# Performance work log

Hardware: AMD Instinct MI355X
Metric: run time of the kernel (lower is better)

## Reference

```python
import jax, jax.numpy as jnp
import numpy as np

B, LQ, LKV = 2, 2048, 1024
DQ = DK = DV_IN = 512
H, DQK, DV = 8, 64, 64
DOUT = 512
SPAN, STRIDE = 128, 2


def setup_inputs() -> dict:
    key = jax.random.key(0)
    ks = jax.random.split(key, 7)
    W_SCALE = 0.05  # keep pre-softmax logits in a sane range
    return {
        "q": jax.random.normal(ks[0], (B, LQ, DQ), jnp.float32),
        "k": jax.random.normal(ks[1], (B, LKV, DK), jnp.float32),
        "v": jax.random.normal(ks[2], (B, LKV, DV_IN), jnp.float32),
        "Wq": jax.random.normal(ks[3], (DQ, H * DQK), jnp.float32) * W_SCALE,
        "Wk": jax.random.normal(ks[4], (DK, H * DQK), jnp.float32) * W_SCALE,
        "Wv": jax.random.normal(ks[5], (DV_IN, H * DV), jnp.float32) * W_SCALE,
        "Wout": jax.random.normal(ks[6], (H * DV, DOUT), jnp.float32) * W_SCALE,
        "head_num": H,
        "span": SPAN,
        "stride": STRIDE,
    }


def reference(q, k, v, Wq, Wk, Wv, Wout, head_num, span, stride):
    batch, length_q, _ = q.shape
    length_kv = k.shape[1]
    width = -(-span // stride)  # ceil(span / stride)
    hd_qk = Wq.shape[1] // head_num
    hd_v = Wv.shape[1] // head_num

    Q = (q @ Wq).reshape(batch, length_q, head_num, hd_qk)
    K = (k @ Wk).reshape(batch, length_kv, head_num, hd_qk)
    V = (v @ Wv).reshape(batch, length_kv, head_num, hd_v)

    # Local-window indices: query j attends kv position j//stride + w - (width-1)
    j = jnp.arange(length_q)[:, None]            # [Lq, 1]
    w = jnp.arange(width)[None, :]               # [1, width]
    orig_col = w - (width - 1) + j // stride     # [Lq, width]
    valid = (orig_col >= 0) & (orig_col < length_kv) & \
            ((j % stride) <= span - 1 - (width - w - 1) * stride)
    mask = jnp.where(valid, 0.0, -jnp.inf).astype(q.dtype)
    idx = jnp.clip(orig_col, 0, length_kv - 1)   # masked entries are dont-care

    Kg = K[:, idx]                               # [B, Lq, width, H, dQK]
    # NOTE: original module applies NO 1/sqrt(d) scaling
    scores = jnp.einsum('bjhd,bjwhd->bhjw', Q, Kg) + mask[None, None]
    p = jax.nn.softmax(scores, axis=-1)          # [B, H, Lq, width]

    Vg = V[:, idx]                               # [B, Lq, width, H, dV]
    out = jnp.einsum('bhjw,bjwhd->bjhd', p, Vg)
    out = out.reshape(batch, length_q, head_num * hd_v)
    return out @ Wout
```

## Files before the change

### kernel.cpp

```cpp
#include <hip/hip_runtime.h>
#include <stdint.h>

typedef _Float16 f16;
typedef _Float16 f16x8 __attribute__((ext_vector_type(8)));
typedef float f32x4 __attribute__((ext_vector_type(4)));

#define LQn   2048
#define LKVn  1024
#define DM    512
#define NH    8

static __device__ __forceinline__ f32x4 mfma_f16(f16x8 a, f16x8 b, f32x4 c) {
  return __builtin_amdgcn_mfma_f32_16x16x32_f16(a, b, c, 0, 0, 0);
}

__global__ __launch_bounds__(256) void transpose_w_kernel(
    const float* __restrict__ Wq, const float* __restrict__ Wk,
    const float* __restrict__ Wv, const float* __restrict__ Wo,
    f16* __restrict__ WT) {
  __shared__ float tile[64 * 65];
  const int bid = blockIdx.x;
  const int mat = bid >> 6;
  const int tb  = bid & 63;
  const int r0 = (tb >> 3) * 64;
  const int c0 = (tb & 7) * 64;
  const float* W = (mat == 0) ? Wq : (mat == 1) ? Wk : (mat == 2) ? Wv : Wo;
  const int t = threadIdx.x;
#pragma unroll
  for (int i = 0; i < 16; ++i) {
    int idx = i * 256 + t;
    int r = idx >> 6, c = idx & 63;
    tile[r * 65 + c] = W[(size_t)(r0 + r) * DM + c0 + c];
  }
  __syncthreads();
#pragma unroll
  for (int i = 0; i < 16; ++i) {
    int idx = i * 256 + t;
    int r = idx >> 6, c = idx & 63;
    WT[(size_t)mat * DM * DM + (size_t)(c0 + r) * DM + r0 + c] =
        (f16)tile[c * 65 + r];
  }
}

__device__ __forceinline__ void proj_tile(const float* __restrict__ Ap,
                                          const f16* __restrict__ Bp,
                                          f16* __restrict__ C,
                                          int m0, int n0,
                                          f16* smA, f16* smB) {
  const int t = threadIdx.x;
  const int lane = t & 63;
  const int w = t >> 6;
  const int ln = lane & 15, hi4 = lane >> 4;
  const int wr = w >> 2, wc = w & 3;
  const f32x4 zf = {0.f, 0.f, 0.f, 0.f};
  f32x4 acc[4][2];
#pragma unroll
  for (int a = 0; a < 4; ++a)
#pragma unroll
    for (int b = 0; b < 2; ++b) acc[a][b] = zf;

  for (int k0 = 0; k0 < 512; k0 += 64) {
    f16x8 av[2], bv[2];
#pragma unroll
    for (int i = 0; i < 2; ++i) {
      int idx = i * 512 + t;
      int r = idx >> 3, u = idx & 7;
      const float* g = Ap + (size_t)(m0 + r) * 512 + k0 + u * 8;
      f32x4 x0 = *(const f32x4*)g, x1 = *(const f32x4*)(g + 4);
      f16x8 hv;
#pragma unroll
      for (int e = 0; e < 4; ++e) { hv[e] = (f16)x0[e]; hv[4 + e] = (f16)x1[e]; }
      av[i] = hv;
      bv[i] = *(const f16x8*)(Bp + (size_t)(n0 + r) * 512 + k0 + u * 8);
    }
    __syncthreads();
#pragma unroll
    for (int i = 0; i < 2; ++i) {
      int idx = i * 512 + t;
      int r = idx >> 3, u = idx & 7;
      int sw = r * 64 + ((u ^ (r & 7)) * 8);
      *(f16x8*)&smA[sw] = av[i];
      *(f16x8*)&smB[sw] = bv[i];
    }
    __syncthreads();
#pragma unroll
    for (int kk = 0; kk < 64; kk += 32) {
      const int ub = kk >> 3;
      f16x8 ah[4], bh[2];
#pragma unroll
      for (int mf = 0; mf < 4; ++mf) {
        int row = wr * 64 + mf * 16 + ln;
        ah[mf] = *(const f16x8*)&smA[row * 64 + (((ub + hi4) ^ (ln & 7)) * 8)];
      }
#pragma unroll
      for (int nf = 0; nf < 2; ++nf) {
        int row = wc * 32 + nf * 16 + ln;
        bh[nf] = *(const f16x8*)&smB[row * 64 + (((ub + hi4) ^ (ln & 7)) * 8)];
      }
#pragma unroll
      for (int mf = 0; mf < 4; ++mf)
#pragma unroll
        for (int nf = 0; nf < 2; ++nf)
          acc[mf][nf] = mfma_f16(ah[mf], bh[nf], acc[mf][nf]);
    }
  }
#pragma unroll
  for (int mf = 0; mf < 4; ++mf)
#pragma unroll
    for (int nf = 0; nf < 2; ++nf)
#pragma unroll
      for (int e = 0; e < 4; ++e) {
        size_t off = (size_t)(m0 + wr * 64 + mf * 16 + hi4 * 4 + e) * 512 +
                     n0 + wc * 32 + nf * 16 + ln;
        C[off] = (f16)acc[mf][nf][e];
      }
}

__global__ __launch_bounds__(512, 2) void proj_kernel(
    const float* __restrict__ q, const float* __restrict__ k,
    const float* __restrict__ v, const f16* __restrict__ WT,
    f16* __restrict__ Qf, f16* __restrict__ Kf, f16* __restrict__ Vf) {
  __shared__ f16 smA[128 * 64];
  __shared__ f16 smB[128 * 64];
  const int bid = blockIdx.x;
  if (bid < 128) {
    int m0 = (bid >> 2) * 128, n0 = (bid & 3) * 128;
    proj_tile(q, WT, Qf, m0, n0, smA, smB);
  } else if (bid < 192) {
    int b2 = bid - 128;
    int m0 = (b2 >> 2) * 128, n0 = (b2 & 3) * 128;
    proj_tile(k, WT + (size_t)DM * DM, Kf, m0, n0, smA, smB);
  } else {
    int b2 = bid - 192;
    int m0 = (b2 >> 2) * 128, n0 = (b2 & 3) * 128;
    proj_tile(v, WT + (size_t)2 * DM * DM, Vf, m0, n0, smA, smB);
  }
}

__global__ __launch_bounds__(256) void outproj_kernel(
    const f16* __restrict__ AO, const f16* __restrict__ Bo,
    float* __restrict__ out) {
  __shared__ f16 smA[64 * 64];
  __shared__ f16 smB[128 * 64];
  const int bid = blockIdx.x;
  const int m0 = (bid >> 2) * 64, n0 = (bid & 3) * 128;
  const int t = threadIdx.x;
  const int lane = t & 63;
  const int w = t >> 6;
  const int ln = lane & 15, hi4 = lane >> 4;
  const f32x4 zf = {0.f, 0.f, 0.f, 0.f};
  f32x4 acc[4][2];
#pragma unroll
  for (int a = 0; a < 4; ++a)
#pragma unroll
    for (int b = 0; b < 2; ++b) acc[a][b] = zf;

  for (int k0 = 0; k0 < 512; k0 += 64) {
    f16x8 av[2], bv[4];
#pragma unroll
    for (int i = 0; i < 2; ++i) {
      int idx = i * 256 + t;
      int r = idx >> 3, u = idx & 7;
      av[i] = *(const f16x8*)(AO + (size_t)(m0 + r) * 512 + k0 + u * 8);
    }
#pragma unroll
    for (int i = 0; i < 4; ++i) {
      int idx = i * 256 + t;
      int r = idx >> 3, u = idx & 7;
      bv[i] = *(const f16x8*)(Bo + (size_t)(n0 + r) * 512 + k0 + u * 8);
    }
    __syncthreads();
#pragma unroll
    for (int i = 0; i < 2; ++i) {
      int idx = i * 256 + t;
      int r = idx >> 3, u = idx & 7;
      *(f16x8*)&smA[r * 64 + ((u ^ (r & 7)) * 8)] = av[i];
    }
#pragma unroll
    for (int i = 0; i < 4; ++i) {
      int idx = i * 256 + t;
      int r = idx >> 3, u = idx & 7;
      *(f16x8*)&smB[r * 64 + ((u ^ (r & 7)) * 8)] = bv[i];
    }
    __syncthreads();
#pragma unroll
    for (int kk = 0; kk < 64; kk += 32) {
      const int ub = kk >> 3;
      f16x8 af[4], bh[2];
#pragma unroll
      for (int mf = 0; mf < 4; ++mf) {
        int row = mf * 16 + ln;
        af[mf] = *(const f16x8*)&smA[row * 64 + (((ub + hi4) ^ (ln & 7)) * 8)];
      }
#pragma unroll
      for (int nf = 0; nf < 2; ++nf) {
        int row = w * 32 + nf * 16 + ln;
        bh[nf] = *(const f16x8*)&smB[row * 64 + (((ub + hi4) ^ (ln & 7)) * 8)];
      }
#pragma unroll
      for (int mf = 0; mf < 4; ++mf)
#pragma unroll
        for (int nf = 0; nf < 2; ++nf)
          acc[mf][nf] = mfma_f16(af[mf], bh[nf], acc[mf][nf]);
    }
  }
#pragma unroll
  for (int mf = 0; mf < 4; ++mf)
#pragma unroll
    for (int nf = 0; nf < 2; ++nf)
#pragma unroll
      for (int e = 0; e < 4; ++e)
        out[(size_t)(m0 + mf * 16 + hi4 * 4 + e) * 512 +
            n0 + w * 32 + nf * 16 + ln] = acc[mf][nf][e];
}

__global__ __launch_bounds__(512, 2) void attn_kernel(
    const f16* __restrict__ Qf, const f16* __restrict__ Kf,
    const f16* __restrict__ Vf, f16* __restrict__ AO) {
  __shared__ f16 smQ[128 * 64];
  __shared__ f16 smK[128 * 64];
  __shared__ f16 smVt[64 * 128];
  __shared__ f16 smP[128 * 128];
  const int bid = blockIdx.x;
  const int qt = bid & 15;
  const int h  = (bid >> 4) & 7;
  const int b  = bid >> 7;
  const int j0 = qt * 128;
  const int pbase = (j0 >> 1) - 63;
  const int t = threadIdx.x;
  const int lane = t & 63, w = t >> 6;
  const int ln = lane & 15, hi4 = lane >> 4;

#pragma unroll
  for (int i = 0; i < 2; ++i) {
    int idx = i * 512 + t;
    int r = idx >> 3, u = idx & 7;
    int sw = r * 64 + ((u ^ (r & 7)) * 8);
    size_t qoff = ((size_t)(b * LQn + j0 + r)) * 512 + h * 64 + u * 8;
    *(f16x8*)&smQ[sw] = *(const f16x8*)(Qf + qoff);
    int p = pbase + r;
    p = p < 0 ? 0 : (p > LKVn - 1 ? LKVn - 1 : p);
    size_t koff = ((size_t)(b * LKVn + p)) * 512 + h * 64 + u * 8;
    *(f16x8*)&smK[sw] = *(const f16x8*)(Kf + koff);
    f16x8 vv = *(const f16x8*)(Vf + koff);
#pragma unroll
    for (int e = 0; e < 8; ++e) {
      int rv = u * 8 + e;
      smVt[rv * 128 + (((r >> 3) ^ (rv & 15)) * 8) + (r & 7)] = vv[e];
    }
  }
  __syncthreads();

  const f32x4 zf = {0.f, 0.f, 0.f, 0.f};
  f32x4 s[8];
#pragma unroll
  for (int cf = 0; cf < 8; ++cf) s[cf] = zf;
#pragma unroll
  for (int kk = 0; kk < 64; kk += 32) {
    const int ub = kk >> 3;
    int addrq = (w * 16 + ln) * 64 + (((ub + hi4) ^ (ln & 7)) * 8);
    f16x8 ah = *(const f16x8*)&smQ[addrq];
#pragma unroll
    for (int cf = 0; cf < 8; ++cf) {
      int addrk = (cf * 16 + ln) * 64 + (((ub + hi4) ^ (ln & 7)) * 8);
      f16x8 bh = *(const f16x8*)&smK[addrk];
      s[cf] = mfma_f16(ah, bh, s[cf]);
    }
  }

#pragma unroll
  for (int r = 0; r < 4; ++r) {
    int rloc = w * 16 + hi4 * 4 + r;
    int wlo = rloc >> 1;
    int colmin = wlo > -pbase ? wlo : -pbase;
    int colmax = wlo + 63;
    float sv[8];
    float mx = -1e30f;
#pragma unroll
    for (int cf = 0; cf < 8; ++cf) {
      int col = cf * 16 + ln;
      float val = s[cf][r];
      bool ok = (col >= colmin) && (col <= colmax);
      sv[cf] = ok ? val : -1e30f;
      mx = fmaxf(mx, sv[cf]);
    }
#pragma unroll
    for (int msk = 1; msk < 16; msk <<= 1) mx = fmaxf(mx, __shfl_xor(mx, msk, 64));
    float sum = 0.f;
#pragma unroll
    for (int cf = 0; cf < 8; ++cf) {
      sv[cf] = __expf(sv[cf] - mx);
      sum += sv[cf];
    }
#pragma unroll
    for (int msk = 1; msk < 16; msk <<= 1) sum += __shfl_xor(sum, msk, 64);
    float rs = 1.0f / sum;
#pragma unroll
    for (int cf = 0; cf < 8; ++cf) {
      int uu = cf * 2 + (ln >> 3);
      smP[rloc * 128 + ((uu ^ (rloc & 15)) * 8) + (ln & 7)] = (f16)(sv[cf] * rs);
    }
  }
  __syncthreads();

  f32x4 o[4];
#pragma unroll
  for (int nf = 0; nf < 4; ++nf) o[nf] = zf;
#pragma unroll
  for (int kk = 0; kk < 128; kk += 32) {
    const int ub = kk >> 3;
    f16x8 pa = *(const f16x8*)&smP[(w * 16 + ln) * 128 + (((ub + hi4) ^ ln) * 8)];
#pragma unroll
    for (int nf = 0; nf < 4; ++nf) {
      int d = nf * 16 + ln;
      f16x8 vf = *(const f16x8*)&smVt[d * 128 + (((ub + hi4) ^ ln) * 8)];
      o[nf] = mfma_f16(pa, vf, o[nf]);
    }
  }

#pragma unroll
  for (int nf = 0; nf < 4; ++nf)
#pragma unroll
    for (int e = 0; e < 4; ++e) {
      int rloc = w * 16 + hi4 * 4 + e;
      AO[((size_t)(b * LQn + j0 + rloc)) * 512 + h * 64 + nf * 16 + ln] =
          (f16)o[nf][e];
    }
}

extern "C" void kernel_launch(void* const* d_in, const int* in_sizes, int n_in,
                              void* d_out, int out_size, void* d_ws, size_t ws_size,
                              hipStream_t stream) {
  const float* q    = (const float*)d_in[0];
  const float* k    = (const float*)d_in[1];
  const float* v    = (const float*)d_in[2];
  const float* Wq   = (const float*)d_in[3];
  const float* Wk   = (const float*)d_in[4];
  const float* Wv   = (const float*)d_in[5];
  const float* Wout = (const float*)d_in[6];
  float* out = (float*)d_out;

  char* ws = (char*)d_ws;
  f16* WT  = (f16*)ws;
  f16* Qf  = (f16*)(ws + (size_t)(2 << 20));
  f16* Kf  = (f16*)(ws + (size_t)(6 << 20));
  f16* Vf  = (f16*)(ws + (size_t)(8 << 20));
  f16* AO  = (f16*)(ws + (size_t)(10 << 20));

  transpose_w_kernel<<<256, 256, 0, stream>>>(Wq, Wk, Wv, Wout, WT);
  proj_kernel<<<256, 512, 0, stream>>>(q, k, v, WT, Qf, Kf, Vf);
  attn_kernel<<<256, 512, 0, stream>>>(Qf, Kf, Vf, AO);
  outproj_kernel<<<256, 256, 0, stream>>>(AO, WT + (size_t)3 * DM * DM, out);
}
```

Before: 41.90 us.

## Pre-swizzle weights into MFMA fragment order and stream them from global memory

The weight transpose kernel now writes weights directly in the per-lane MFMA B-fragment layout. The projection and output-projection GEMMs load full-K row strips of the activation into LDS once, then stream weight fragments straight from global or L2 into registers with a two-deep prefetch. This removes the weight staging through shared memory and the per-k-step barriers. The cost is that each block rereads the full 512x512 weight matrix from L2, and tiles are now tall and thin (32 or 16 rows by 512 columns) instead of 128x128.

```diff
diff --git a/kernel.cpp b/kernel.cpp
--- a/kernel.cpp
+++ b/kernel.cpp
@@ -9,6 +9,7 @@
 #define LKVn  1024
 #define DM    512
 #define NH    8
+#define WSZ   262144
 
 static __device__ __forceinline__ f32x4 mfma_f16(f16x8 a, f16x8 b, f32x4 c) {
   return __builtin_amdgcn_mfma_f32_16x16x32_f16(a, b, c, 0, 0, 0);
@@ -17,7 +18,7 @@
 __global__ __launch_bounds__(256) void transpose_w_kernel(
     const float* __restrict__ Wq, const float* __restrict__ Wk,
     const float* __restrict__ Wv, const float* __restrict__ Wo,
-    f16* __restrict__ WT) {
+    f16* __restrict__ WTf) {
   __shared__ float tile[64 * 65];
   const int bid = blockIdx.x;
   const int mat = bid >> 6;
@@ -37,181 +38,161 @@
   for (int i = 0; i < 16; ++i) {
     int idx = i * 256 + t;
     int r = idx >> 6, c = idx & 63;
-    WT[(size_t)mat * DM * DM + (size_t)(c0 + r) * DM + r0 + c] =
+    int n = c0 + r, kk = r0 + c;
+    int n16 = n >> 4, ln = n & 15;
+    int it = kk >> 5, h4 = (kk >> 3) & 3, e = kk & 7;
+    int lane = h4 * 16 + ln;
+    WTf[(size_t)mat * WSZ + ((size_t)(n16 * 16 + it) * 64 + lane) * 8 + e] =
         (f16)tile[c * 65 + r];
   }
 }
 
-__device__ __forceinline__ void proj_tile(const float* __restrict__ Ap,
-                                          const f16* __restrict__ Bp,
-                                          f16* __restrict__ C,
-                                          int m0, int n0,
-                                          f16* smA, f16* smB) {
+__global__ __launch_bounds__(512) void proj_kernel(
+    const float* __restrict__ q, const float* __restrict__ k,
+    const float* __restrict__ v, const f16* __restrict__ WTf,
+    f16* __restrict__ Qf, f16* __restrict__ Kf, f16* __restrict__ Vf) {
+  __shared__ f16 smA[32 * 512];
+  const int bid = blockIdx.x;
+  const float* A;
+  const f16* Bf;
+  f16* C;
+  int m0;
+  if (bid < 128)      { A = q; Bf = WTf;            C = Qf; m0 = bid * 32; }
+  else if (bid < 192) { A = k; Bf = WTf + WSZ;      C = Kf; m0 = (bid - 128) * 32; }
+  else                { A = v; Bf = WTf + 2 * WSZ;  C = Vf; m0 = (bid - 192) * 32; }
+
   const int t = threadIdx.x;
   const int lane = t & 63;
   const int w = t >> 6;
   const int ln = lane & 15, hi4 = lane >> 4;
-  const int wr = w >> 2, wc = w & 3;
+
+#pragma unroll
+  for (int i = 0; i < 4; ++i) {
+    int idx = i * 512 + t;
+    int r = idx >> 6, u = idx & 63;
+    const float* g = A + (size_t)(m0 + r) * 512 + u * 8;
+    f32x4 x0 = *(const f32x4*)g, x1 = *(const f32x4*)(g + 4);
+    f16x8 hv;
+#pragma unroll
+    for (int e = 0; e < 4; ++e) { hv[e] = (f16)x0[e]; hv[4 + e] = (f16)x1[e]; }
+    int phys = (u & ~7) | ((u & 7) ^ (r & 7));
+    *(f16x8*)&smA[r * 512 + phys * 8] = hv;
+  }
+  __syncthreads();
+
+  const f16* gB = Bf + ((size_t)(w * 4) * 16 * 64 + lane) * 8;
   const f32x4 zf = {0.f, 0.f, 0.f, 0.f};
-  f32x4 acc[4][2];
-#pragma unroll
-  for (int a = 0; a < 4; ++a)
-#pragma unroll
-    for (int b = 0; b < 2; ++b) acc[a][b] = zf;
-
-  for (int k0 = 0; k0 < 512; k0 += 64) {
-    f16x8 av[2], bv[2];
-#pragma unroll
-    for (int i = 0; i < 2; ++i) {
-      int idx = i * 512 + t;
-      int r = idx >> 3, u = idx & 7;
-      const float* g = Ap + (size_t)(m0 + r) * 512 + k0 + u * 8;
-      f32x4 x0 = *(const f32x4*)g, x1 = *(const f32x4*)(g + 4);
-      f16x8 hv;
-#pragma unroll
-      for (int e = 0; e < 4; ++e) { hv[e] = (f16)x0[e]; hv[4 + e] = (f16)x1[e]; }
-      av[i] = hv;
-      bv[i] = *(const f16x8*)(Bp + (size_t)(n0 + r) * 512 + k0 + u * 8);
-    }
-    __syncthreads();
-#pragma unroll
-    for (int i = 0; i < 2; ++i) {
-      int idx = i * 512 + t;
-      int r = idx >> 3, u = idx & 7;
-      int sw = r * 64 + ((u ^ (r & 7)) * 8);
-      *(f16x8*)&smA[sw] = av[i];
-      *(f16x8*)&smB[sw] = bv[i];
-    }
-    __syncthreads();
-#pragma unroll
-    for (int kk = 0; kk < 64; kk += 32) {
-      const int ub = kk >> 3;
-      f16x8 ah[4], bh[2];
-#pragma unroll
-      for (int mf = 0; mf < 4; ++mf) {
-        int row = wr * 64 + mf * 16 + ln;
-        ah[mf] = *(const f16x8*)&smA[row * 64 + (((ub + hi4) ^ (ln & 7)) * 8)];
+  f32x4 acc[2][4];
+#pragma unroll
+  for (int a = 0; a < 2; ++a)
+#pragma unroll
+    for (int b = 0; b < 4; ++b) acc[a][b] = zf;
+
+  f16x8 buf0[4], buf1[4];
+#pragma unroll
+  for (int nf = 0; nf < 4; ++nf) buf0[nf] = *(const f16x8*)(gB + nf * 8192);
+#pragma unroll
+  for (int nf = 0; nf < 4; ++nf) buf1[nf] = *(const f16x8*)(gB + nf * 8192 + 512);
+
+#pragma unroll
+  for (int it = 0; it < 16; ++it) {
+    f16x8 bfr[4], ah[2];
+#pragma unroll
+    for (int nf = 0; nf < 4; ++nf) bfr[nf] = (it & 1) ? buf1[nf] : buf0[nf];
+    if (it + 2 < 16) {
+#pragma unroll
+      for (int nf = 0; nf < 4; ++nf) {
+        f16x8 nv = *(const f16x8*)(gB + nf * 8192 + (it + 2) * 512);
+        if (it & 1) buf1[nf] = nv; else buf0[nf] = nv;
       }
-#pragma unroll
-      for (int nf = 0; nf < 2; ++nf) {
-        int row = wc * 32 + nf * 16 + ln;
-        bh[nf] = *(const f16x8*)&smB[row * 64 + (((ub + hi4) ^ (ln & 7)) * 8)];
-      }
-#pragma unroll
-      for (int mf = 0; mf < 4; ++mf)
-#pragma unroll
-        for (int nf = 0; nf < 2; ++nf)
-          acc[mf][nf] = mfma_f16(ah[mf], bh[nf], acc[mf][nf]);
-    }
-  }
-#pragma unroll
-  for (int mf = 0; mf < 4; ++mf)
-#pragma unroll
-    for (int nf = 0; nf < 2; ++nf)
+    }
+#pragma unroll
+    for (int mf = 0; mf < 2; ++mf) {
+      int row = mf * 16 + ln;
+      int uu = it * 4 + hi4;
+      int phys = (uu & ~7) | ((uu & 7) ^ (row & 7));
+      ah[mf] = *(const f16x8*)&smA[row * 512 + phys * 8];
+    }
+#pragma unroll
+    for (int mf = 0; mf < 2; ++mf)
+#pragma unroll
+      for (int nf = 0; nf < 4; ++nf)
+        acc[mf][nf] = mfma_f16(ah[mf], bfr[nf], acc[mf][nf]);
+  }
+
+#pragma unroll
+  for (int mf = 0; mf < 2; ++mf)
+#pragma unroll
+    for (int nf = 0; nf < 4; ++nf)
 #pragma unroll
       for (int e = 0; e < 4; ++e) {
-        size_t off = (size_t)(m0 + wr * 64 + mf * 16 + hi4 * 4 + e) * 512 +
-                     n0 + wc * 32 + nf * 16 + ln;
+        size_t off = (size_t)(m0 + mf * 16 + hi4 * 4 + e) * 512 +
+                     w * 64 + nf * 16 + ln;
         C[off] = (f16)acc[mf][nf][e];
       }
 }
 
-__global__ __launch_bounds__(512, 2) void proj_kernel(
-    const float* __restrict__ q, const float* __restrict__ k,
-    const float* __restrict__ v, const f16* __restrict__ WT,
-    f16* __restrict__ Qf, f16* __restrict__ Kf, f16* __restrict__ Vf) {
-  __shared__ f16 smA[128 * 64];
-  __shared__ f16 smB[128 * 64];
+__global__ __launch_bounds__(512) void outproj_kernel(
+    const f16* __restrict__ AO, const f16* __restrict__ WTf,
+    float* __restrict__ out) {
+  __shared__ f16 smA[16 * 512];
   const int bid = blockIdx.x;
-  if (bid < 128) {
-    int m0 = (bid >> 2) * 128, n0 = (bid & 3) * 128;
-    proj_tile(q, WT, Qf, m0, n0, smA, smB);
-  } else if (bid < 192) {
-    int b2 = bid - 128;
-    int m0 = (b2 >> 2) * 128, n0 = (b2 & 3) * 128;
-    proj_tile(k, WT + (size_t)DM * DM, Kf, m0, n0, smA, smB);
-  } else {
-    int b2 = bid - 192;
-    int m0 = (b2 >> 2) * 128, n0 = (b2 & 3) * 128;
-    proj_tile(v, WT + (size_t)2 * DM * DM, Vf, m0, n0, smA, smB);
-  }
-}
-
-__global__ __launch_bounds__(256) void outproj_kernel(
-    const f16* __restrict__ AO, const f16* __restrict__ Bo,
-    float* __restrict__ out) {
-  __shared__ f16 smA[64 * 64];
-  __shared__ f16 smB[128 * 64];
-  const int bid = blockIdx.x;
-  const int m0 = (bid >> 2) * 64, n0 = (bid & 3) * 128;
+  const int m0 = bid * 16;
+  const f16* Bf = WTf + (size_t)3 * WSZ;
   const int t = threadIdx.x;
   const int lane = t & 63;
   const int w = t >> 6;
   const int ln = lane & 15, hi4 = lane >> 4;
+
+#pragma unroll
+  for (int i = 0; i < 2; ++i) {
+    int idx = i * 512 + t;
+    int r = idx >> 6, u = idx & 63;
+    f16x8 hv = *(const f16x8*)(AO + (size_t)(m0 + r) * 512 + u * 8);
+    int phys = (u & ~7) | ((u & 7) ^ (r & 7));
+    *(f16x8*)&smA[r * 512 + phys * 8] = hv;
+  }
+  __syncthreads();
+
+  const f16* gB = Bf + ((size_t)(w * 4) * 16 * 64 + lane) * 8;
   const f32x4 zf = {0.f, 0.f, 0.f, 0.f};
-  f32x4 acc[4][2];
-#pragma unroll
-  for (int a = 0; a < 4; ++a)
-#pragma unroll
-    for (int b = 0; b < 2; ++b) acc[a][b] = zf;
-
-  for (int k0 = 0; k0 < 512; k0 += 64) {
-    f16x8 av[2], bv[4];
-#pragma unroll
-    for (int i = 0; i < 2; ++i) {
-      int idx = i * 256 + t;
-      int r = idx >> 3, u = idx & 7;
-      av[i] = *(const f16x8*)(AO + (size_t)(m0 + r) * 512 + k0 + u * 8);
-    }
-#pragma unroll
-    for (int i = 0; i < 4; ++i) {
-      int idx = i * 256 + t;
-      int r = idx >> 3, u = idx & 7;
-      bv[i] = *(const f16x8*)(Bo + (size_t)(n0 + r) * 512 + k0 + u * 8);
-    }
-    __syncthreads();
-#pragma unroll
-    for (int i = 0; i < 2; ++i) {
-      int idx = i * 256 + t;
-      int r = idx >> 3, u = idx & 7;
-      *(f16x8*)&smA[r * 64 + ((u ^ (r & 7)) * 8)] = av[i];
-    }
-#pragma unroll
-    for (int i = 0; i < 4; ++i) {
-      int idx = i * 256 + t;
-      int r = idx >> 3, u = idx & 7;
-      *(f16x8*)&smB[r * 64 + ((u ^ (r & 7)) * 8)] = bv[i];
-    }
-    __syncthreads();
-#pragma unroll
-    for (int kk = 0; kk < 64; kk += 32) {
-      const int ub = kk >> 3;
-      f16x8 af[4], bh[2];
-#pragma unroll
-      for (int mf = 0; mf < 4; ++mf) {
-        int row = mf * 16 + ln;
-        af[mf] = *(const f16x8*)&smA[row * 64 + (((ub + hi4) ^ (ln & 7)) * 8)];
+  f32x4 acc[4];
+#pragma unroll
+  for (int b = 0; b < 4; ++b) acc[b] = zf;
+
+  f16x8 buf0[4], buf1[4];
+#pragma unroll
+  for (int nf = 0; nf < 4; ++nf) buf0[nf] = *(const f16x8*)(gB + nf * 8192);
+#pragma unroll
+  for (int nf = 0; nf < 4; ++nf) buf1[nf] = *(const f16x8*)(gB + nf * 8192 + 512);
+
+#pragma unroll
+  for (int it = 0; it < 16; ++it) {
+    f16x8 bfr[4], av;
+#pragma unroll
+    for (int nf = 0; nf < 4; ++nf) bfr[nf] = (it & 1) ? buf1[nf] : buf0[nf];
+    if (it + 2 < 16) {
+#pragma unroll
+      for (int nf = 0; nf < 4; ++nf) {
+        f16x8 nv = *(const f16x8*)(gB + nf * 8192 + (it + 2) * 512);
+        if (it & 1) buf1[nf] = nv; else buf0[nf] = nv;
       }
-#pragma unroll
-      for (int nf = 0; nf < 2; ++nf) {
-        int row = w * 32 + nf * 16 + ln;
-        bh[nf] = *(const f16x8*)&smB[row * 64 + (((ub + hi4) ^ (ln & 7)) * 8)];
-      }
-#pragma unroll
-      for (int mf = 0; mf < 4; ++mf)
-#pragma unroll
-        for (int nf = 0; nf < 2; ++nf)
-          acc[mf][nf] = mfma_f16(af[mf], bh[nf], acc[mf][nf]);
-    }
-  }
-#pragma unroll
-  for (int mf = 0; mf < 4; ++mf)
-#pragma unroll
-    for (int nf = 0; nf < 2; ++nf)
-#pragma unroll
-      for (int e = 0; e < 4; ++e)
-        out[(size_t)(m0 + mf * 16 + hi4 * 4 + e) * 512 +
-            n0 + w * 32 + nf * 16 + ln] = acc[mf][nf][e];
+    }
+    {
+      int uu = it * 4 + hi4;
+      int phys = (uu & ~7) | ((uu & 7) ^ (ln & 7));
+      av = *(const f16x8*)&smA[ln * 512 + phys * 8];
+    }
+#pragma unroll
+    for (int nf = 0; nf < 4; ++nf)
+      acc[nf] = mfma_f16(av, bfr[nf], acc[nf]);
+  }
+
+#pragma unroll
+  for (int nf = 0; nf < 4; ++nf)
+#pragma unroll
+    for (int e = 0; e < 4; ++e)
+      out[(size_t)(m0 + hi4 * 4 + e) * 512 + w * 64 + nf * 16 + ln] = acc[nf][e];
 }
 
 __global__ __launch_bounds__(512, 2) void attn_kernel(
@@ -341,14 +322,14 @@
   float* out = (float*)d_out;
 
   char* ws = (char*)d_ws;
-  f16* WT  = (f16*)ws;
+  f16* WTf = (f16*)ws;
   f16* Qf  = (f16*)(ws + (size_t)(2 << 20));
   f16* Kf  = (f16*)(ws + (size_t)(6 << 20));
   f16* Vf  = (f16*)(ws + (size_t)(8 << 20));
   f16* AO  = (f16*)(ws + (size_t)(10 << 20));
 
-  transpose_w_kernel<<<256, 256, 0, stream>>>(Wq, Wk, Wv, Wout, WT);
-  proj_kernel<<<256, 512, 0, stream>>>(q, k, v, WT, Qf, Kf, Vf);
+  transpose_w_kernel<<<256, 256, 0, stream>>>(Wq, Wk, Wv, Wout, WTf);
+  proj_kernel<<<256, 512, 0, stream>>>(q, k, v, WTf, Qf, Kf, Vf);
   attn_kernel<<<256, 512, 0, stream>>>(Qf, Kf, Vf, AO);
-  outproj_kernel<<<256, 256, 0, stream>>>(AO, WT + (size_t)3 * DM * DM, out);
-}
+  outproj_kernel<<<256, 512, 0, stream>>>(AO, WTf, out);
+}
```

New measurement: 39.44 us. 1.06x faster.
